# Kernel optimization log

Hardware: AMD Instinct MI355X
Metric: run time of the kernel (lower is better)

## Reference

```python
import jax, jax.numpy as jnp
import numpy as np


def setup_inputs() -> dict:
    key = jax.random.key(0)
    ks = jax.random.split(key, 7)
    C = 256
    Cqk = C // 8  # 32
    B, D, H, W = 4, 16, 16, 16
    s_in = 1.0 / np.sqrt(C)  # conv1x1 fan_in = C
    return {
        "x": jax.random.normal(ks[0], (B, C, D, H, W), dtype=jnp.float32),
        "Wq": jax.random.uniform(ks[1], (Cqk, C), jnp.float32, -s_in, s_in),
        "bq": jax.random.uniform(ks[2], (Cqk,), jnp.float32, -s_in, s_in),
        "Wk": jax.random.uniform(ks[3], (Cqk, C), jnp.float32, -s_in, s_in),
        "bk": jax.random.uniform(ks[4], (Cqk,), jnp.float32, -s_in, s_in),
        "Wv": jax.random.uniform(ks[5], (C, C), jnp.float32, -s_in, s_in),
        "bv": jax.random.uniform(ks[6], (C,), jnp.float32, -s_in, s_in),
    }


def reference(x, Wq, bq, Wk, bk, Wv, bv):
    B, C, D, H, W = x.shape
    N = D * H * W
    xf = x.reshape(B, C, N)  # [B, C, N]
    # 1x1x1 convs == per-voxel GEMMs over the channel dim
    q = jnp.einsum('oc,bcn->bon', Wq, xf) + bq[None, :, None]  # [B, Cqk, N]
    k = jnp.einsum('oc,bcn->bon', Wk, xf) + bk[None, :, None]  # [B, Cqk, N]
    v = jnp.einsum('oc,bcn->bon', Wv, xf) + bv[None, :, None]  # [B, C, N]
    # attention[b, n, m] = softmax_m( q[:, n] . k[:, m] )
    scores = jnp.einsum('bcn,bcm->bnm', q, k)  # [B, N, N]
    attn = jax.nn.softmax(scores, axis=-1)
    # out = value @ attention^T  -> out[b, c, n] = sum_m v[b,c,m] * attn[b,n,m]
    out = jnp.einsum('bcm,bnm->bcn', v, attn)
    return x + out.reshape(B, C, D, H, W)
```

## Files before the change

kernel.cpp:

```cpp
#include <hip/hip_runtime.h>
#include <math.h>

#define B_   4
#define C_   256
#define CQK  32
#define N_   4096
#define TQ   64
#define TM   64
#define HITERS ((N_ / 2) / TM)
#define PSS  72
#define XTS  264

typedef __attribute__((ext_vector_type(8))) short short8;
typedef __attribute__((ext_vector_type(4))) short short4v;
typedef __attribute__((ext_vector_type(4))) float f32x4;
typedef __attribute__((ext_vector_type(2))) unsigned int uint2v;

#if __has_builtin(__builtin_amdgcn_exp2f)
#define EXP2F(x) __builtin_amdgcn_exp2f(x)
#else
#define EXP2F(x) exp2f(x)
#endif

__device__ __forceinline__ unsigned short f2bf(float f) {
    unsigned u = __builtin_bit_cast(unsigned, f);
    u += 0x7fffu + ((u >> 16) & 1u);
    return (unsigned short)(u >> 16);
}
__device__ __forceinline__ float bf2f(unsigned short s) {
    return __builtin_bit_cast(float, (unsigned)s << 16);
}
__device__ __forceinline__ unsigned pack2bf(float a, float b) {
    unsigned ua = __builtin_bit_cast(unsigned, a) + 0x8000u;
    unsigned ub = __builtin_bit_cast(unsigned, b) + 0x8000u;
#if __has_builtin(__builtin_amdgcn_perm)
    return __builtin_amdgcn_perm(ub, ua, 0x07060302u);
#else
    return (ua >> 16) | (ub & 0xffff0000u);
#endif
}

__global__ __launch_bounds__(256) void cvt_w(
    const float* __restrict__ Wq, const float* __restrict__ bq,
    const float* __restrict__ Wk, const float* __restrict__ bk,
    const float* __restrict__ Wv, const float* __restrict__ bv,
    unsigned short* __restrict__ wbf, float* __restrict__ biasf)
{
    const float LOG2E = 1.4426950408889634f;
    const int r = blockIdx.x;
    const int t = threadIdx.x;
    const float* src = (r < 32) ? (Wq + r * C_)
                     : (r < 64) ? (Wk + (r - 32) * C_)
                                : (Wv + (r - 64) * C_);
    const float scale = (r < 32) ? LOG2E : 1.0f;
    wbf[r * C_ + t] = f2bf(src[t] * scale);
    if (t == 0)
        biasf[r] = (r < 32) ? bq[r] * LOG2E : (r < 64) ? bk[r - 32] : bv[r - 64];
}

__global__ __launch_bounds__(256, 2) void proj_qkv(
    const float* __restrict__ x, const unsigned short* __restrict__ wbf,
    const float* __restrict__ biasf,
    unsigned short* __restrict__ qb, unsigned short* __restrict__ kb,
    unsigned short* __restrict__ vb)
{
    __shared__ __align__(16) unsigned short xT[64 * XTS];
    __shared__ __align__(16) unsigned short qks[64 * 72];

    const int t    = threadIdx.x;
    const int w    = t >> 6;
    const int lane = t & 63;
    const int quad = lane >> 4;
    const int c16  = lane & 15;
    const int n0   = blockIdx.x * 64;
    const int b    = blockIdx.y;

#pragma unroll
    for (int p = 0; p < 16; ++p) {
        const int c  = (t >> 2) + 64 * (p >> 2);
        const int nq = (t & 3) + 4 * (p & 3);
        const f32x4 xv = *(const f32x4*)&x[((size_t)(b * C_) + c) * N_ + n0 + 4 * nq];
#pragma unroll
        for (int j = 0; j < 4; ++j)
            xT[(4 * nq + j) * XTS + c] = f2bf(xv[j]);
    }
    __syncthreads();

    f32x4 acc[5][4];
#pragma unroll
    for (int i = 0; i < 5; ++i)
#pragma unroll
        for (int nt = 0; nt < 4; ++nt) acc[i][nt] = (f32x4){0.f, 0.f, 0.f, 0.f};

    const unsigned short* wr = wbf + (size_t)(80 * w + c16) * C_ + quad * 8;

#pragma unroll
    for (int ks = 0; ks < 8; ++ks) {
        short8 af[5], bf[4];
#pragma unroll
        for (int i = 0; i < 5; ++i)
            af[i] = *(const short8*)(wr + (size_t)(16 * i) * C_ + 32 * ks);
#pragma unroll
        for (int nt = 0; nt < 4; ++nt)
            bf[nt] = *(const short8*)&xT[(16 * nt + c16) * XTS + ks * 32 + quad * 8];
#pragma unroll
        for (int i = 0; i < 5; ++i)
#pragma unroll
            for (int nt = 0; nt < 4; ++nt)
                acc[i][nt] = __builtin_amdgcn_mfma_f32_16x16x32_bf16(af[i], bf[nt], acc[i][nt], 0, 0, 0);
    }

#pragma unroll
    for (int i = 0; i < 5; ++i) {
        const int OT = 5 * w + i;
        const int obase = OT * 16 + 4 * quad;
        const f32x4 bv4 = *(const f32x4*)&biasf[obase];
#pragma unroll
        for (int nt = 0; nt < 4; ++nt) {
            const int n = n0 + 16 * nt + c16;
            float vals[4];
#pragma unroll
            for (int r = 0; r < 4; ++r) vals[r] = acc[i][nt][r] + bv4[r];
            if (OT >= 4) {
#pragma unroll
                for (int r = 0; r < 4; ++r)
                    vb[((size_t)(b * C_) + obase + r - 64) * N_ + n] = f2bf(vals[r]);
            } else {
                const int row = 16 * nt + c16;
                const int col = (OT < 2 ? 0 : 32) + (OT & 1) * 16 + 4 * quad;
                short4v pk;
#pragma unroll
                for (int r = 0; r < 4; ++r) pk[r] = (short)f2bf(vals[r]);
                *(short4v*)&qks[row * 72 + col] = pk;
            }
        }
    }
    __syncthreads();
    if (w < 2) {
        unsigned short* dst = w ? kb : qb;
        const int coff = w ? 32 : 0;
#pragma unroll
        for (int h = 0; h < 4; ++h) {
            const int n = 16 * h + (lane >> 2);
            const int c = (lane & 3) * 8;
            const short8 v = *(const short8*)&qks[n * 72 + coff + c];
            *(short8*)(dst + ((size_t)(b * N_) + n0 + n) * 32 + c) = v;
        }
    }
}

__global__ __launch_bounds__(512, 4) void attn_kernel(
    const unsigned short* __restrict__ qg,
    const unsigned short* __restrict__ kg,
    const unsigned short* __restrict__ vg,
    float* __restrict__ outp,
    unsigned short* __restrict__ Op1,
    float* __restrict__ lp)
{
    __shared__ __align__(16) unsigned short ks[TM * 40];
    __shared__ __align__(16) unsigned short vs[C_ * TM];
    __shared__ __align__(16) unsigned short ps[TQ * PSS];
    __shared__ float ls[4 * TQ];

    const int t    = threadIdx.x;
    const int w    = t >> 6;
    const int lane = t & 63;
    const int quad = lane >> 4;
    const int c16  = lane & 15;
    const int flat = blockIdx.x;
    const int half = flat & 1;
    const int b    = (flat >> 1) & 3;
    const int q0   = (flat >> 3) * TQ;
    const int kvb0 = half * (N_ / 2);
    const int f   = w & 3;
    const int qg_ = w >> 2;
    const int cs = w & 3;
    const int pg = w >> 2;

    const unsigned short* kbase = kg + (size_t)(b * N_) * 32;
    const unsigned short* vbase = vg + (size_t)(b * C_) * N_;

    short8 bq[2];
#pragma unroll
    for (int g = 0; g < 2; ++g)
        bq[g] = *(const short8*)(qg + ((size_t)(b * N_) + q0 + 16 * (2 * qg_ + g) + c16) * 32 + quad * 8);

    const int vc0 = t >> 3, vj = t & 7;
    const int kn = t >> 2, kseg = t & 3;

    short8 vpre[4], kpre;
#pragma unroll
    for (int p = 0; p < 4; ++p)
        vpre[p] = *(const short8*)(vbase + (size_t)(vc0 + 64 * p) * N_ + kvb0 + vj * 8);
    if (t < 256)
        kpre = *(const short8*)(kbase + (size_t)(kvb0 + kn) * 32 + kseg * 8);

    f32x4 O[4][2];
#pragma unroll
    for (int ct = 0; ct < 4; ++ct)
#pragma unroll
        for (int qt = 0; qt < 2; ++qt) O[ct][qt] = (f32x4){0.f, 0.f, 0.f, 0.f};

    float lacc[2] = {0.f, 0.f};

#pragma unroll 1
    for (int it = 0; it < HITERS; ++it) {
#pragma unroll
        for (int p = 0; p < 4; ++p) {
            const int c = vc0 + 64 * p;
            *(short8*)&vs[c * TM + 8 * (vj ^ (c & 7))] = vpre[p];
        }
        if (t < 256)
            *(short8*)&ks[kn * 40 + kseg * 8] = kpre;
        __syncthreads();

        const short8 ak = *(const short8*)&ks[(16 * f + c16) * 40 + quad * 8];
        const f32x4 z = {0.f, 0.f, 0.f, 0.f};
        f32x4 sf[2];
#pragma unroll
        for (int g = 0; g < 2; ++g)
            sf[g] = __builtin_amdgcn_mfma_f32_16x16x32_bf16(ak, bq[g], z, 0, 0, 0);

#pragma unroll
        for (int g = 0; g < 2; ++g) {
            float p[4];
#pragma unroll
            for (int r = 0; r < 4; ++r) p[r] = EXP2F(sf[g][r]);
            lacc[g] += (p[0] + p[1]) + (p[2] + p[3]);
            uint2v u;
            u.x = pack2bf(p[0], p[1]);
            u.y = pack2bf(p[2], p[3]);
            *(uint2v*)&ps[(16 * (2 * qg_ + g) + c16) * PSS + f * 16 + 4 * quad] = u;
        }
        __syncthreads();

        if (it < HITERS - 1) {
            const int kv0n = kvb0 + (it + 1) * TM;
#pragma unroll
            for (int p = 0; p < 4; ++p)
                vpre[p] = *(const short8*)(vbase + (size_t)(vc0 + 64 * p) * N_ + kv0n + vj * 8);
            if (t < 256)
                kpre = *(const short8*)(kbase + (size_t)(kv0n + kn) * 32 + kseg * 8);
        }

        short8 bp[2][2];
#pragma unroll
        for (int qt = 0; qt < 2; ++qt)
#pragma unroll
            for (int s = 0; s < 2; ++s)
                bp[qt][s] = *(const short8*)&ps[(32 * pg + 16 * qt + c16) * PSS + 32 * s + 8 * quad];
#pragma unroll
        for (int s = 0; s < 2; ++s)
#pragma unroll
            for (int ct = 0; ct < 4; ++ct) {
                const int c = 64 * cs + 16 * ct + c16;
                const short8 av = *(const short8*)&vs[c * TM + 8 * ((4 * s + quad) ^ (c & 7))];
#pragma unroll
                for (int qt = 0; qt < 2; ++qt)
                    O[ct][qt] = __builtin_amdgcn_mfma_f32_16x16x32_bf16(av, bp[qt][s], O[ct][qt], 0, 0, 0);
            }
        __syncthreads();
    }

#pragma unroll
    for (int g = 0; g < 2; ++g) {
        lacc[g] += __shfl_xor(lacc[g], 16);
        lacc[g] += __shfl_xor(lacc[g], 32);
    }
    if (quad == 0) {
#pragma unroll
        for (int g = 0; g < 2; ++g)
            ls[f * TQ + 16 * (2 * qg_ + g) + c16] = lacc[g];
    }
    __syncthreads();

    if (half == 0) {
        float* ob = outp + (size_t)(b * C_) * N_;
#pragma unroll
        for (int ct = 0; ct < 4; ++ct)
#pragma unroll
            for (int qt = 0; qt < 2; ++qt) {
                const int n = q0 + 32 * pg + 16 * qt + c16;
#pragma unroll
                for (int r = 0; r < 4; ++r) {
                    const int c = 64 * cs + 16 * ct + 4 * quad + r;
                    ob[(size_t)c * N_ + n] = O[ct][qt][r];
                }
            }
    } else {
        unsigned short* ob = Op1 + (size_t)(b * C_) * N_;
#pragma unroll
        for (int ct = 0; ct < 4; ++ct)
#pragma unroll
            for (int qt = 0; qt < 2; ++qt) {
                const int n = q0 + 32 * pg + 16 * qt + c16;
#pragma unroll
                for (int r = 0; r < 4; ++r) {
                    const int c = 64 * cs + 16 * ct + 4 * quad + r;
                    ob[(size_t)c * N_ + n] = f2bf(O[ct][qt][r]);
                }
            }
    }
    if (w == 0) {
        const int qq = lane;
        const float lv = ls[qq] + ls[TQ + qq] + ls[2 * TQ + qq] + ls[3 * TQ + qq];
        lp[(size_t)(half * B_ + b) * N_ + q0 + qq] = lv;
    }
}

__global__ __launch_bounds__(256) void combine_kernel(
    const float* __restrict__ x,
    const unsigned short* __restrict__ Op1,
    const float* __restrict__ lp,
    float* __restrict__ out)
{
    __shared__ float linv[1024];

    const int t  = threadIdx.x;
    const int n0 = blockIdx.x * 1024;
    const int c0 = blockIdx.y * 8;
    const int b  = blockIdx.z;

#pragma unroll
    for (int i = 0; i < 4; ++i) {
        const int n = n0 + t + 256 * i;
        const float l = lp[(size_t)b * N_ + n] + lp[(size_t)(B_ + b) * N_ + n];
        linv[t + 256 * i] = 1.0f / l;
    }
    __syncthreads();

#pragma unroll
    for (int cc = 0; cc < 8; ++cc) {
        const int c = c0 + cc;
        const size_t base = ((size_t)(b * C_) + c) * N_ + n0 + 4 * t;
        const f32x4 o0 = *(const f32x4*)&out[base];
        const short4v a1 = *(const short4v*)&Op1[base];
        const f32x4 xv = *(const f32x4*)&x[base];
        f32x4 o;
        o.x = xv.x + (o0.x + bf2f((unsigned short)a1[0])) * linv[4 * t + 0];
        o.y = xv.y + (o0.y + bf2f((unsigned short)a1[1])) * linv[4 * t + 1];
        o.z = xv.z + (o0.z + bf2f((unsigned short)a1[2])) * linv[4 * t + 2];
        o.w = xv.w + (o0.w + bf2f((unsigned short)a1[3])) * linv[4 * t + 3];
        *(f32x4*)&out[base] = o;
    }
}

extern "C" void kernel_launch(void* const* d_in, const int* in_sizes, int n_in,
                              void* d_out, int out_size, void* d_ws, size_t ws_size,
                              hipStream_t stream) {
    const float* x  = (const float*)d_in[0];
    const float* Wq = (const float*)d_in[1];
    const float* bq = (const float*)d_in[2];
    const float* Wk = (const float*)d_in[3];
    const float* bk = (const float*)d_in[4];
    const float* Wv = (const float*)d_in[5];
    const float* bv = (const float*)d_in[6];
    float* out = (float*)d_out;

    unsigned short* ws16 = (unsigned short*)d_ws;
    unsigned short* qb  = ws16;
    unsigned short* kb  = qb + (size_t)B_ * N_ * 32;
    unsigned short* vb  = kb + (size_t)B_ * N_ * 32;
    unsigned short* Op1 = vb + (size_t)B_ * C_ * N_;
    unsigned short* wbf = Op1 + (size_t)B_ * C_ * N_;
    float* biasf = (float*)(wbf + 320 * C_);
    float* lpp   = biasf + 320;

    cvt_w<<<dim3(320), 256, 0, stream>>>(Wq, bq, Wk, bk, Wv, bv, wbf, biasf);
    proj_qkv<<<dim3(N_ / 64, B_), 256, 0, stream>>>(x, wbf, biasf, qb, kb, vb);
    attn_kernel<<<dim3(512), 512, 0, stream>>>(qb, kb, vb, out, Op1, lpp);
    combine_kernel<<<dim3(4, 32, B_), 256, 0, stream>>>(x, Op1, lpp, out);
}
```

Baseline: 154.3 us.

## Drop split-KV and combine kernel; fuse normalization and residual into attention

The attention kernel no longer splits the key/value range across two blocks. Each block now walks the full sequence with 128-wide KV tiles and applies the softmax normalisation and residual add directly in its epilogue. This removes the separate combine kernel, the bf16 partial-output buffer and the partial-sum buffer, along with their extra global traffic. In exchange the grid halves to 256 blocks of 512 threads, so parallelism and occupancy are lower, and the larger LDS tiles limit blocks per CU.

```diff
diff --git a/kernel.cpp b/kernel.cpp
--- a/kernel.cpp
+++ b/kernel.cpp
@@ -6,9 +6,9 @@
 #define CQK  32
 #define N_   4096
 #define TQ   64
-#define TM   64
-#define HITERS ((N_ / 2) / TM)
-#define PSS  72
+#define TM   128
+#define HIT2 (N_ / TM)
+#define PSS  136
 #define XTS  264
 
 typedef __attribute__((ext_vector_type(8))) short short8;
@@ -149,18 +149,18 @@
     }
 }
 
-__global__ __launch_bounds__(512, 4) void attn_kernel(
+__global__ __launch_bounds__(512, 2) void attn_kernel(
     const unsigned short* __restrict__ qg,
     const unsigned short* __restrict__ kg,
     const unsigned short* __restrict__ vg,
-    float* __restrict__ outp,
-    unsigned short* __restrict__ Op1,
-    float* __restrict__ lp)
+    const float* __restrict__ x,
+    float* __restrict__ out)
 {
     __shared__ __align__(16) unsigned short ks[TM * 40];
     __shared__ __align__(16) unsigned short vs[C_ * TM];
     __shared__ __align__(16) unsigned short ps[TQ * PSS];
-    __shared__ float ls[4 * TQ];
+    __shared__ float ls[8 * TQ];
+    __shared__ float linv[TQ];
 
     const int t    = threadIdx.x;
     const int w    = t >> 6;
@@ -168,32 +168,27 @@
     const int quad = lane >> 4;
     const int c16  = lane & 15;
     const int flat = blockIdx.x;
-    const int half = flat & 1;
-    const int b    = (flat >> 1) & 3;
-    const int q0   = (flat >> 3) * TQ;
-    const int kvb0 = half * (N_ / 2);
-    const int f   = w & 3;
-    const int qg_ = w >> 2;
+    const int b    = flat & 3;
+    const int q0   = (flat >> 2) * TQ;
     const int cs = w & 3;
     const int pg = w >> 2;
 
     const unsigned short* kbase = kg + (size_t)(b * N_) * 32;
     const unsigned short* vbase = vg + (size_t)(b * C_) * N_;
 
-    short8 bq[2];
-#pragma unroll
-    for (int g = 0; g < 2; ++g)
-        bq[g] = *(const short8*)(qg + ((size_t)(b * N_) + q0 + 16 * (2 * qg_ + g) + c16) * 32 + quad * 8);
-
-    const int vc0 = t >> 3, vj = t & 7;
+    short8 bq[4];
+#pragma unroll
+    for (int g = 0; g < 4; ++g)
+        bq[g] = *(const short8*)(qg + ((size_t)(b * N_) + q0 + 16 * g + c16) * 32 + quad * 8);
+
+    const int vcr = t >> 4, vj = t & 15;
     const int kn = t >> 2, kseg = t & 3;
 
-    short8 vpre[4], kpre;
-#pragma unroll
-    for (int p = 0; p < 4; ++p)
-        vpre[p] = *(const short8*)(vbase + (size_t)(vc0 + 64 * p) * N_ + kvb0 + vj * 8);
-    if (t < 256)
-        kpre = *(const short8*)(kbase + (size_t)(kvb0 + kn) * 32 + kseg * 8);
+    short8 vpre[8], kpre;
+#pragma unroll
+    for (int p = 0; p < 8; ++p)
+        vpre[p] = *(const short8*)(vbase + (size_t)(vcr + 32 * p) * N_ + vj * 8);
+    kpre = *(const short8*)(kbase + (size_t)kn * 32 + kseg * 8);
 
     f32x4 O[4][2];
 #pragma unroll
@@ -201,28 +196,27 @@
 #pragma unroll
         for (int qt = 0; qt < 2; ++qt) O[ct][qt] = (f32x4){0.f, 0.f, 0.f, 0.f};
 
-    float lacc[2] = {0.f, 0.f};
+    float lacc[4] = {0.f, 0.f, 0.f, 0.f};
 
 #pragma unroll 1
-    for (int it = 0; it < HITERS; ++it) {
-#pragma unroll
-        for (int p = 0; p < 4; ++p) {
-            const int c = vc0 + 64 * p;
-            *(short8*)&vs[c * TM + 8 * (vj ^ (c & 7))] = vpre[p];
-        }
-        if (t < 256)
-            *(short8*)&ks[kn * 40 + kseg * 8] = kpre;
+    for (int it = 0; it < HIT2; ++it) {
+#pragma unroll
+        for (int p = 0; p < 8; ++p) {
+            const int c = vcr + 32 * p;
+            *(short8*)&vs[c * TM + 8 * (vj ^ (c & 15))] = vpre[p];
+        }
+        *(short8*)&ks[kn * 40 + kseg * 8] = kpre;
         __syncthreads();
 
-        const short8 ak = *(const short8*)&ks[(16 * f + c16) * 40 + quad * 8];
+        const short8 ak = *(const short8*)&ks[(16 * w + c16) * 40 + quad * 8];
         const f32x4 z = {0.f, 0.f, 0.f, 0.f};
-        f32x4 sf[2];
-#pragma unroll
-        for (int g = 0; g < 2; ++g)
+        f32x4 sf[4];
+#pragma unroll
+        for (int g = 0; g < 4; ++g)
             sf[g] = __builtin_amdgcn_mfma_f32_16x16x32_bf16(ak, bq[g], z, 0, 0, 0);
 
 #pragma unroll
-        for (int g = 0; g < 2; ++g) {
+        for (int g = 0; g < 4; ++g) {
             float p[4];
 #pragma unroll
             for (int r = 0; r < 4; ++r) p[r] = EXP2F(sf[g][r]);
@@ -230,31 +224,30 @@
             uint2v u;
             u.x = pack2bf(p[0], p[1]);
             u.y = pack2bf(p[2], p[3]);
-            *(uint2v*)&ps[(16 * (2 * qg_ + g) + c16) * PSS + f * 16 + 4 * quad] = u;
+            *(uint2v*)&ps[(16 * g + c16) * PSS + w * 16 + 4 * quad] = u;
         }
         __syncthreads();
 
-        if (it < HITERS - 1) {
-            const int kv0n = kvb0 + (it + 1) * TM;
-#pragma unroll
-            for (int p = 0; p < 4; ++p)
-                vpre[p] = *(const short8*)(vbase + (size_t)(vc0 + 64 * p) * N_ + kv0n + vj * 8);
-            if (t < 256)
-                kpre = *(const short8*)(kbase + (size_t)(kv0n + kn) * 32 + kseg * 8);
-        }
-
-        short8 bp[2][2];
+        if (it < HIT2 - 1) {
+            const int kv0n = (it + 1) * TM;
+#pragma unroll
+            for (int p = 0; p < 8; ++p)
+                vpre[p] = *(const short8*)(vbase + (size_t)(vcr + 32 * p) * N_ + kv0n + vj * 8);
+            kpre = *(const short8*)(kbase + (size_t)(kv0n + kn) * 32 + kseg * 8);
+        }
+
+        short8 bp[2][4];
 #pragma unroll
         for (int qt = 0; qt < 2; ++qt)
 #pragma unroll
-            for (int s = 0; s < 2; ++s)
+            for (int s = 0; s < 4; ++s)
                 bp[qt][s] = *(const short8*)&ps[(32 * pg + 16 * qt + c16) * PSS + 32 * s + 8 * quad];
 #pragma unroll
-        for (int s = 0; s < 2; ++s)
+        for (int s = 0; s < 4; ++s)
 #pragma unroll
             for (int ct = 0; ct < 4; ++ct) {
                 const int c = 64 * cs + 16 * ct + c16;
-                const short8 av = *(const short8*)&vs[c * TM + 8 * ((4 * s + quad) ^ (c & 7))];
+                const short8 av = *(const short8*)&vs[c * TM + 8 * ((4 * s + quad) ^ (c & 15))];
 #pragma unroll
                 for (int qt = 0; qt < 2; ++qt)
                     O[ct][qt] = __builtin_amdgcn_mfma_f32_16x16x32_bf16(av, bp[qt][s], O[ct][qt], 0, 0, 0);
@@ -263,86 +256,41 @@
     }
 
 #pragma unroll
-    for (int g = 0; g < 2; ++g) {
+    for (int g = 0; g < 4; ++g) {
         lacc[g] += __shfl_xor(lacc[g], 16);
         lacc[g] += __shfl_xor(lacc[g], 32);
     }
     if (quad == 0) {
 #pragma unroll
-        for (int g = 0; g < 2; ++g)
-            ls[f * TQ + 16 * (2 * qg_ + g) + c16] = lacc[g];
+        for (int g = 0; g < 4; ++g)
+            ls[w * TQ + 16 * g + c16] = lacc[g];
     }
     __syncthreads();
-
-    if (half == 0) {
-        float* ob = outp + (size_t)(b * C_) * N_;
-#pragma unroll
-        for (int ct = 0; ct < 4; ++ct)
-#pragma unroll
-            for (int qt = 0; qt < 2; ++qt) {
-                const int n = q0 + 32 * pg + 16 * qt + c16;
-#pragma unroll
-                for (int r = 0; r < 4; ++r) {
-                    const int c = 64 * cs + 16 * ct + 4 * quad + r;
-                    ob[(size_t)c * N_ + n] = O[ct][qt][r];
-                }
+    if (w == 0) {
+        float s = 0.f;
+#pragma unroll
+        for (int j = 0; j < 8; ++j) s += ls[j * TQ + lane];
+        linv[lane] = 1.0f / s;
+    }
+    __syncthreads();
+
+    const float* xb = x + (size_t)(b * C_) * N_;
+    float* ob = out + (size_t)(b * C_) * N_;
+    float li[2];
+#pragma unroll
+    for (int qt = 0; qt < 2; ++qt) li[qt] = linv[32 * pg + 16 * qt + c16];
+#pragma unroll
+    for (int ct = 0; ct < 4; ++ct)
+#pragma unroll
+        for (int qt = 0; qt < 2; ++qt) {
+            const int n = q0 + 32 * pg + 16 * qt + c16;
+#pragma unroll
+            for (int r = 0; r < 4; ++r) {
+                const int c = 64 * cs + 16 * ct + 4 * quad + r;
+                const size_t idx = (size_t)c * N_ + n;
+                ob[idx] = xb[idx] + O[ct][qt][r] * li[qt];
             }
-    } else {
-        unsigned short* ob = Op1 + (size_t)(b * C_) * N_;
-#pragma unroll
-        for (int ct = 0; ct < 4; ++ct)
-#pragma unroll
-            for (int qt = 0; qt < 2; ++qt) {
-                const int n = q0 + 32 * pg + 16 * qt + c16;
-#pragma unroll
-                for (int r = 0; r < 4; ++r) {
-                    const int c = 64 * cs + 16 * ct + 4 * quad + r;
-                    ob[(size_t)c * N_ + n] = f2bf(O[ct][qt][r]);
-                }
-            }
-    }
-    if (w == 0) {
-        const int qq = lane;
-        const float lv = ls[qq] + ls[TQ + qq] + ls[2 * TQ + qq] + ls[3 * TQ + qq];
-        lp[(size_t)(half * B_ + b) * N_ + q0 + qq] = lv;
-    }
-}
-
-__global__ __launch_bounds__(256) void combine_kernel(
-    const float* __restrict__ x,
-    const unsigned short* __restrict__ Op1,
-    const float* __restrict__ lp,
-    float* __restrict__ out)
-{
-    __shared__ float linv[1024];
-
-    const int t  = threadIdx.x;
-    const int n0 = blockIdx.x * 1024;
-    const int c0 = blockIdx.y * 8;
-    const int b  = blockIdx.z;
-
-#pragma unroll
-    for (int i = 0; i < 4; ++i) {
-        const int n = n0 + t + 256 * i;
-        const float l = lp[(size_t)b * N_ + n] + lp[(size_t)(B_ + b) * N_ + n];
-        linv[t + 256 * i] = 1.0f / l;
-    }
-    __syncthreads();
-
-#pragma unroll
-    for (int cc = 0; cc < 8; ++cc) {
-        const int c = c0 + cc;
-        const size_t base = ((size_t)(b * C_) + c) * N_ + n0 + 4 * t;
-        const f32x4 o0 = *(const f32x4*)&out[base];
-        const short4v a1 = *(const short4v*)&Op1[base];
-        const f32x4 xv = *(const f32x4*)&x[base];
-        f32x4 o;
-        o.x = xv.x + (o0.x + bf2f((unsigned short)a1[0])) * linv[4 * t + 0];
-        o.y = xv.y + (o0.y + bf2f((unsigned short)a1[1])) * linv[4 * t + 1];
-        o.z = xv.z + (o0.z + bf2f((unsigned short)a1[2])) * linv[4 * t + 2];
-        o.w = xv.w + (o0.w + bf2f((unsigned short)a1[3])) * linv[4 * t + 3];
-        *(f32x4*)&out[base] = o;
-    }
+        }
 }
 
 extern "C" void kernel_launch(void* const* d_in, const int* in_sizes, int n_in,
@@ -361,13 +309,10 @@
     unsigned short* qb  = ws16;
     unsigned short* kb  = qb + (size_t)B_ * N_ * 32;
     unsigned short* vb  = kb + (size_t)B_ * N_ * 32;
-    unsigned short* Op1 = vb + (size_t)B_ * C_ * N_;
-    unsigned short* wbf = Op1 + (size_t)B_ * C_ * N_;
+    unsigned short* wbf = vb + (size_t)B_ * C_ * N_;
     float* biasf = (float*)(wbf + 320 * C_);
-    float* lpp   = biasf + 320;
 
     cvt_w<<<dim3(320), 256, 0, stream>>>(Wq, bq, Wk, bk, Wv, bv, wbf, biasf);
     proj_qkv<<<dim3(N_ / 64, B_), 256, 0, stream>>>(x, wbf, biasf, qb, kb, vb);
-    attn_kernel<<<dim3(512), 512, 0, stream>>>(qb, kb, vb, out, Op1, lpp);
-    combine_kernel<<<dim3(4, 32, B_), 256, 0, stream>>>(x, Op1, lpp, out);
-}
+    attn_kernel<<<dim3(256), 512, 0, stream>>>(qb, kb, vb, x, out);
+}
```

Result: no change. 154.6 us (+0.2%).

## Double-buffer V/K register prefetch two tiles ahead and use lighter barriers

Applied to the files above, without the earlier changes.

The main attention loop is unrolled by two with two register prefetch buffers, so global loads for V and K tiles are issued two iterations ahead instead of one, giving more latency hiding. __syncthreads is replaced by an inline-asm barrier that waits only on LDS counters, so outstanding global loads do not block at barriers. This costs extra VGPRs (another 5 short8 per thread), which may pressure occupancy under launch_bounds(512,4).

```diff
diff --git a/kernel.cpp b/kernel.cpp
--- a/kernel.cpp
+++ b/kernel.cpp
@@ -21,6 +21,8 @@
 #else
 #define EXP2F(x) exp2f(x)
 #endif
+
+#define BAR() asm volatile("s_waitcnt lgkmcnt(0)\n\ts_barrier" ::: "memory")
 
 __device__ __forceinline__ unsigned short f2bf(float f) {
     unsigned u = __builtin_bit_cast(unsigned, f);
@@ -149,6 +151,60 @@
     }
 }
 
+#define ATTN_STEP(VP, KP, PFC, DOPF)                                                      \
+  {                                                                                       \
+    _Pragma("unroll")                                                                     \
+    for (int p = 0; p < 4; ++p) {                                                         \
+      const int c = vc0 + 64 * p;                                                         \
+      *(short8*)&vs[c * TM + 8 * (vj ^ (c & 7))] = VP[p];                                 \
+    }                                                                                     \
+    if (t < 256)                                                                          \
+      *(short8*)&ks[kn * 40 + kseg * 8] = KP;                                             \
+    BAR();                                                             \
+    const short8 ak = *(const short8*)&ks[(16 * f + c16) * 40 + quad * 8];                \
+    const f32x4 zz = {0.f, 0.f, 0.f, 0.f};                                                \
+    const f32x4 sf0 = __builtin_amdgcn_mfma_f32_16x16x32_bf16(ak, bq[0], zz, 0, 0, 0);    \
+    const f32x4 sf1 = __builtin_amdgcn_mfma_f32_16x16x32_bf16(ak, bq[1], zz, 0, 0, 0);    \
+    {                                                                                     \
+      float p0[4], p1[4];                                                                 \
+      _Pragma("unroll")                                                                   \
+      for (int r = 0; r < 4; ++r) { p0[r] = EXP2F(sf0[r]); p1[r] = EXP2F(sf1[r]); }       \
+      lacc[0] += (p0[0] + p0[1]) + (p0[2] + p0[3]);                                       \
+      lacc[1] += (p1[0] + p1[1]) + (p1[2] + p1[3]);                                       \
+      uint2v u0, u1;                                                                      \
+      u0.x = pack2bf(p0[0], p0[1]); u0.y = pack2bf(p0[2], p0[3]);                         \
+      u1.x = pack2bf(p1[0], p1[1]); u1.y = pack2bf(p1[2], p1[3]);                         \
+      *(uint2v*)&ps[(16 * (2 * qg_ + 0) + c16) * PSS + f * 16 + 4 * quad] = u0;           \
+      *(uint2v*)&ps[(16 * (2 * qg_ + 1) + c16) * PSS + f * 16 + 4 * quad] = u1;           \
+    }                                                                                     \
+    BAR();                                                              \
+    if (DOPF) {                                                                           \
+      const int kv0n = kvb0 + (PFC) * TM;                                                 \
+      _Pragma("unroll")                                                                   \
+      for (int p = 0; p < 4; ++p)                                                         \
+        VP[p] = *(const short8*)(vbase + (size_t)(vc0 + 64 * p) * N_ + kv0n + vj * 8);    \
+      if (t < 256)                                                                        \
+        KP = *(const short8*)(kbase + (size_t)(kv0n + kn) * 32 + kseg * 8);               \
+    }                                                                                     \
+    short8 bp[2][2];                                                                      \
+    _Pragma("unroll")                                                                     \
+    for (int qt = 0; qt < 2; ++qt)                                                        \
+      _Pragma("unroll")                                                                   \
+      for (int s = 0; s < 2; ++s)                                                         \
+        bp[qt][s] = *(const short8*)&ps[(32 * pg + 16 * qt + c16) * PSS + 32 * s + 8 * quad]; \
+    _Pragma("unroll")                                                                     \
+    for (int s = 0; s < 2; ++s)                                                           \
+      _Pragma("unroll")                                                                   \
+      for (int ct = 0; ct < 4; ++ct) {                                                    \
+        const int c = 64 * cs + 16 * ct + c16;                                            \
+        const short8 av = *(const short8*)&vs[c * TM + 8 * ((4 * s + quad) ^ (c & 7))];   \
+        _Pragma("unroll")                                                                 \
+        for (int qt = 0; qt < 2; ++qt)                                                    \
+          O[ct][qt] = __builtin_amdgcn_mfma_f32_16x16x32_bf16(av, bp[qt][s], O[ct][qt], 0, 0, 0); \
+      }                                                                                   \
+    BAR();                                   \
+  }
+
 __global__ __launch_bounds__(512, 4) void attn_kernel(
     const unsigned short* __restrict__ qg,
     const unsigned short* __restrict__ kg,
@@ -188,12 +244,16 @@
     const int vc0 = t >> 3, vj = t & 7;
     const int kn = t >> 2, kseg = t & 3;
 
-    short8 vpre[4], kpre;
-#pragma unroll
-    for (int p = 0; p < 4; ++p)
-        vpre[p] = *(const short8*)(vbase + (size_t)(vc0 + 64 * p) * N_ + kvb0 + vj * 8);
-    if (t < 256)
-        kpre = *(const short8*)(kbase + (size_t)(kvb0 + kn) * 32 + kseg * 8);
+    short8 vpA[4], vpB[4], kpA, kpB;
+#pragma unroll
+    for (int p = 0; p < 4; ++p) {
+        vpA[p] = *(const short8*)(vbase + (size_t)(vc0 + 64 * p) * N_ + kvb0 + vj * 8);
+        vpB[p] = *(const short8*)(vbase + (size_t)(vc0 + 64 * p) * N_ + kvb0 + TM + vj * 8);
+    }
+    if (t < 256) {
+        kpA = *(const short8*)(kbase + (size_t)(kvb0 + kn) * 32 + kseg * 8);
+        kpB = *(const short8*)(kbase + (size_t)(kvb0 + TM + kn) * 32 + kseg * 8);
+    }
 
     f32x4 O[4][2];
 #pragma unroll
@@ -204,62 +264,10 @@
     float lacc[2] = {0.f, 0.f};
 
 #pragma unroll 1
-    for (int it = 0; it < HITERS; ++it) {
-#pragma unroll
-        for (int p = 0; p < 4; ++p) {
-            const int c = vc0 + 64 * p;
-            *(short8*)&vs[c * TM + 8 * (vj ^ (c & 7))] = vpre[p];
-        }
-        if (t < 256)
-            *(short8*)&ks[kn * 40 + kseg * 8] = kpre;
-        __syncthreads();
-
-        const short8 ak = *(const short8*)&ks[(16 * f + c16) * 40 + quad * 8];
-        const f32x4 z = {0.f, 0.f, 0.f, 0.f};
-        f32x4 sf[2];
-#pragma unroll
-        for (int g = 0; g < 2; ++g)
-            sf[g] = __builtin_amdgcn_mfma_f32_16x16x32_bf16(ak, bq[g], z, 0, 0, 0);
-
-#pragma unroll
-        for (int g = 0; g < 2; ++g) {
-            float p[4];
-#pragma unroll
-            for (int r = 0; r < 4; ++r) p[r] = EXP2F(sf[g][r]);
-            lacc[g] += (p[0] + p[1]) + (p[2] + p[3]);
-            uint2v u;
-            u.x = pack2bf(p[0], p[1]);
-            u.y = pack2bf(p[2], p[3]);
-            *(uint2v*)&ps[(16 * (2 * qg_ + g) + c16) * PSS + f * 16 + 4 * quad] = u;
-        }
-        __syncthreads();
-
-        if (it < HITERS - 1) {
-            const int kv0n = kvb0 + (it + 1) * TM;
-#pragma unroll
-            for (int p = 0; p < 4; ++p)
-                vpre[p] = *(const short8*)(vbase + (size_t)(vc0 + 64 * p) * N_ + kv0n + vj * 8);
-            if (t < 256)
-                kpre = *(const short8*)(kbase + (size_t)(kv0n + kn) * 32 + kseg * 8);
-        }
-
-        short8 bp[2][2];
-#pragma unroll
-        for (int qt = 0; qt < 2; ++qt)
-#pragma unroll
-            for (int s = 0; s < 2; ++s)
-                bp[qt][s] = *(const short8*)&ps[(32 * pg + 16 * qt + c16) * PSS + 32 * s + 8 * quad];
-#pragma unroll
-        for (int s = 0; s < 2; ++s)
-#pragma unroll
-            for (int ct = 0; ct < 4; ++ct) {
-                const int c = 64 * cs + 16 * ct + c16;
-                const short8 av = *(const short8*)&vs[c * TM + 8 * ((4 * s + quad) ^ (c & 7))];
-#pragma unroll
-                for (int qt = 0; qt < 2; ++qt)
-                    O[ct][qt] = __builtin_amdgcn_mfma_f32_16x16x32_bf16(av, bp[qt][s], O[ct][qt], 0, 0, 0);
-            }
-        __syncthreads();
+    for (int it2 = 0; it2 < HITERS / 2; ++it2) {
+        const bool dopf = (it2 < HITERS / 2 - 1);
+        ATTN_STEP(vpA, kpA, 2 * it2 + 2, dopf)
+        ATTN_STEP(vpB, kpB, 2 * it2 + 3, dopf)
     }
 
 #pragma unroll
```

After: 155.4 us. No clear change (+0.7%).

## Halve projection tile, vectorize x transpose, stage V output through LDS

Applied to the files above, without the earlier changes.

The QKV projection kernel now handles 32 voxels per block instead of 64, which doubles the grid to 512 blocks. The x load is restructured so each thread packs 8 channels into a 16-byte LDS store instead of writing scalar bf16 values. V results are staged in shared memory and written to global memory as coalesced 16-byte rows, replacing scattered 2-byte stores. In exchange, each block reuses the weight fragments over half as many columns, so global weight reads per output roughly double.

```diff
diff --git a/kernel.cpp b/kernel.cpp
--- a/kernel.cpp
+++ b/kernel.cpp
@@ -9,7 +9,8 @@
 #define TM   64
 #define HITERS ((N_ / 2) / TM)
 #define PSS  72
-#define XTS  264
+#define XT2  264
+#define VOS  40
 
 typedef __attribute__((ext_vector_type(8))) short short8;
 typedef __attribute__((ext_vector_type(4))) short short4v;
@@ -64,49 +65,56 @@
     unsigned short* __restrict__ qb, unsigned short* __restrict__ kb,
     unsigned short* __restrict__ vb)
 {
-    __shared__ __align__(16) unsigned short xT[64 * XTS];
-    __shared__ __align__(16) unsigned short qks[64 * 72];
+    __shared__ __align__(16) unsigned short xT[32 * XT2];
+    __shared__ __align__(16) unsigned short vout[256 * VOS];
+    __shared__ __align__(16) unsigned short qks[32 * 72];
 
     const int t    = threadIdx.x;
     const int w    = t >> 6;
     const int lane = t & 63;
     const int quad = lane >> 4;
     const int c16  = lane & 15;
-    const int n0   = blockIdx.x * 64;
+    const int n0   = blockIdx.x * 32;
     const int b    = blockIdx.y;
 
-#pragma unroll
-    for (int p = 0; p < 16; ++p) {
-        const int c  = (t >> 2) + 64 * (p >> 2);
-        const int nq = (t & 3) + 4 * (p & 3);
-        const f32x4 xv = *(const f32x4*)&x[((size_t)(b * C_) + c) * N_ + n0 + 4 * nq];
-#pragma unroll
-        for (int j = 0; j < 4; ++j)
-            xT[(4 * nq + j) * XTS + c] = f2bf(xv[j]);
+    {
+        const int c0 = (t >> 3) * 8;
+        const int nq = t & 7;
+        f32x4 xv[8];
+#pragma unroll
+        for (int i = 0; i < 8; ++i)
+            xv[i] = *(const f32x4*)&x[((size_t)(b * C_) + c0 + i) * N_ + n0 + 4 * nq];
+#pragma unroll
+        for (int j = 0; j < 4; ++j) {
+            short8 pk;
+#pragma unroll
+            for (int i = 0; i < 8; ++i) pk[i] = (short)f2bf(xv[i][j]);
+            *(short8*)&xT[(4 * nq + j) * XT2 + c0] = pk;
+        }
     }
     __syncthreads();
 
-    f32x4 acc[5][4];
+    f32x4 acc[5][2];
 #pragma unroll
     for (int i = 0; i < 5; ++i)
 #pragma unroll
-        for (int nt = 0; nt < 4; ++nt) acc[i][nt] = (f32x4){0.f, 0.f, 0.f, 0.f};
+        for (int nt = 0; nt < 2; ++nt) acc[i][nt] = (f32x4){0.f, 0.f, 0.f, 0.f};
 
     const unsigned short* wr = wbf + (size_t)(80 * w + c16) * C_ + quad * 8;
 
 #pragma unroll
     for (int ks = 0; ks < 8; ++ks) {
-        short8 af[5], bf[4];
+        short8 af[5], bf[2];
 #pragma unroll
         for (int i = 0; i < 5; ++i)
             af[i] = *(const short8*)(wr + (size_t)(16 * i) * C_ + 32 * ks);
 #pragma unroll
-        for (int nt = 0; nt < 4; ++nt)
-            bf[nt] = *(const short8*)&xT[(16 * nt + c16) * XTS + ks * 32 + quad * 8];
+        for (int nt = 0; nt < 2; ++nt)
+            bf[nt] = *(const short8*)&xT[(16 * nt + c16) * XT2 + ks * 32 + quad * 8];
 #pragma unroll
         for (int i = 0; i < 5; ++i)
 #pragma unroll
-            for (int nt = 0; nt < 4; ++nt)
+            for (int nt = 0; nt < 2; ++nt)
                 acc[i][nt] = __builtin_amdgcn_mfma_f32_16x16x32_bf16(af[i], bf[nt], acc[i][nt], 0, 0, 0);
     }
 
@@ -116,31 +124,38 @@
         const int obase = OT * 16 + 4 * quad;
         const f32x4 bv4 = *(const f32x4*)&biasf[obase];
 #pragma unroll
-        for (int nt = 0; nt < 4; ++nt) {
-            const int n = n0 + 16 * nt + c16;
+        for (int nt = 0; nt < 2; ++nt) {
+            const int n = 16 * nt + c16;
             float vals[4];
 #pragma unroll
             for (int r = 0; r < 4; ++r) vals[r] = acc[i][nt][r] + bv4[r];
             if (OT >= 4) {
 #pragma unroll
                 for (int r = 0; r < 4; ++r)
-                    vb[((size_t)(b * C_) + obase + r - 64) * N_ + n] = f2bf(vals[r]);
+                    vout[(obase + r - 64) * VOS + n] = f2bf(vals[r]);
             } else {
-                const int row = 16 * nt + c16;
                 const int col = (OT < 2 ? 0 : 32) + (OT & 1) * 16 + 4 * quad;
                 short4v pk;
 #pragma unroll
                 for (int r = 0; r < 4; ++r) pk[r] = (short)f2bf(vals[r]);
-                *(short4v*)&qks[row * 72 + col] = pk;
+                *(short4v*)&qks[n * 72 + col] = pk;
             }
         }
     }
     __syncthreads();
+
+#pragma unroll
+    for (int p = 0; p < 4; ++p) {
+        const int c   = 64 * p + (t >> 2);
+        const int seg = t & 3;
+        const short8 vv = *(const short8*)&vout[c * VOS + seg * 8];
+        *(short8*)(vb + ((size_t)(b * C_) + c) * N_ + n0 + seg * 8) = vv;
+    }
     if (w < 2) {
         unsigned short* dst = w ? kb : qb;
         const int coff = w ? 32 : 0;
 #pragma unroll
-        for (int h = 0; h < 4; ++h) {
+        for (int h = 0; h < 2; ++h) {
             const int n = 16 * h + (lane >> 2);
             const int c = (lane & 3) * 8;
             const short8 v = *(const short8*)&qks[n * 72 + coff + c];
@@ -367,7 +382,7 @@
     float* lpp   = biasf + 320;
 
     cvt_w<<<dim3(320), 256, 0, stream>>>(Wq, bq, Wk, bk, Wv, bv, wbf, biasf);
-    proj_qkv<<<dim3(N_ / 64, B_), 256, 0, stream>>>(x, wbf, biasf, qb, kb, vb);
+    proj_qkv<<<dim3(N_ / 32, B_), 256, 0, stream>>>(x, wbf, biasf, qb, kb, vb);
     attn_kernel<<<dim3(512), 512, 0, stream>>>(qb, kb, vb, out, Op1, lpp);
     combine_kernel<<<dim3(4, 32, B_), 256, 0, stream>>>(x, Op1, lpp, out);
 }
```

After: 156.1 us. Within noise of the previous version (+1.2%).
